# Kernel tuning notes

Measured on AMD Instinct MI355X. Metric: run time of the kernel, lower is better.

Reference implementation:

```python
import jax, jax.numpy as jnp
import numpy as np

N = 20000   # nodes
M = 20000   # hyperedges
E = 400000  # incidences
F = 256     # raw feature dim (exact_num_feature_dim)
HID = 256   # hidden
HEADS = 4
FS = HID // HEADS  # factor_size
OUT = 128


def setup_inputs() -> dict:
    key = jax.random.key(0)
    k = jax.random.split(key, 5)
    x = jax.random.normal(k[0], (N, F), jnp.float32)
    edge_index = jax.random.randint(k[1], (2, E), 0, M)  # row0: node idx, row1: hyperedge idx
    edge_weight = jax.random.uniform(k[2], (E,), jnp.float32)
    W_enc = jax.random.normal(k[3], (F, HID), jnp.float32) / np.sqrt(F).astype(np.float32)
    W_cls = jax.random.normal(k[4], (F * HEADS, OUT), jnp.float32) / np.sqrt(F * HEADS).astype(np.float32)
    return {"x": x, "edge_weight": edge_weight, "W_enc": W_enc, "W_cls": W_cls,
            "edge_index": edge_index}


def _segment_mean(vals, idx, num):
    # mean-aggregate rows of vals into `num` segments (torch get_xe_by_mean_agg)
    s = jax.ops.segment_sum(vals, idx, num_segments=num)
    c = jax.ops.segment_sum(jnp.ones((idx.shape[0], 1), vals.dtype), idx, num_segments=num)
    return s / jnp.maximum(c, 1.0)


def reference(x, edge_weight, W_enc, W_cls, edge_index):
    src = edge_index[0]  # node index per incidence
    he = edge_index[1]   # hyperedge index per incidence
    x0 = x

    # encoder + per-head softmax over factor dim (dropout is identity in eval mode)
    h = (x @ W_enc).reshape(N, HEADS, FS)
    h = jax.nn.softmax(h, axis=-1).reshape(N, HEADS * FS)

    # hyperedge embeddings = mean of member-node embeddings
    h_gather = h[src]                                    # [E, HID]
    temp_edge = _segment_mean(h_gather, he, M).reshape(M, HEADS, FS)
    temp_x = h_gather.reshape(E, HEADS, FS)

    # elementwise attention score per incidence, scatter-min per hyperedge
    att_calc = (temp_edge[he] * temp_x).sum(-1)          # [E, HEADS]
    att_score = jnp.full((M, HEADS), jnp.inf, h.dtype).at[he].min(att_calc)
    att_score = jnp.where(jnp.isinf(att_score), jnp.zeros((), h.dtype), att_score)

    # disentanglement factor loss
    gram = jnp.einsum('mhf,mgf->mhg', temp_edge, temp_edge)  # [M, HEADS, HEADS]
    factor_loss = (-(temp_edge * temp_edge).sum(-1) + jax.nn.logsumexp(gram, axis=-1)).mean()

    # propagation layer: node->hyperedge mean of raw feats, per-head attention scale,
    # then hyperedge->node mean; concat heads -> [N, HEADS*F]
    xe = _segment_mean(x0[src], he, M)                   # [M, F]
    xe_h = att_score[:, :, None] * xe[:, None, :]        # [M, HEADS, F]
    x_out = _segment_mean(xe_h[he].reshape(E, HEADS * F), src, N)  # [N, HEADS*F]

    logits = x_out @ W_cls                               # [N, OUT]
    return logits, factor_loss
```

## Files before the change

kernel.cpp:

```cpp
#include <hip/hip_runtime.h>
#include <hip/hip_fp16.h>

#define N_NODES 20000
#define M_EDGES 20000
#define E_INC   400000
#define HE_CACHE 8

__device__ __forceinline__ unsigned char f2e5(float f) {
  unsigned short u = __half_as_ushort(__float2half_rn(f));
  u = (unsigned short)(u + 0x7F + ((u >> 8) & 1));
  return (unsigned char)(u >> 8);
}
__device__ __forceinline__ float e52f(unsigned b) {
  return __half2float(__ushort_as_half((unsigned short)(b << 8)));
}
__device__ __forceinline__ float4 e5x4(unsigned p) {
  float4 r;
  r.x = e52f(p & 0xFFu);  r.y = e52f((p >> 8) & 0xFFu);
  r.z = e52f((p >> 16) & 0xFFu);  r.w = e52f(p >> 24);
  return r;
}

__global__ __launch_bounds__(256) void encode_kernel(
    const float* __restrict__ x, const float* __restrict__ Wenc,
    unsigned char* __restrict__ hx)
{
  __shared__ float xs[16][256];
  const int n0 = blockIdx.x * 16;
  const int t = threadIdx.x;
  #pragma unroll
  for (int r = 0; r < 16; ++r) xs[r][t] = x[(size_t)(n0 + r) * 256 + t];
  __syncthreads();

  float acc[16];
  #pragma unroll
  for (int r = 0; r < 16; ++r) acc[r] = 0.f;
  for (int k = 0; k < 256; k += 4) {
    float w0 = Wenc[(size_t)(k+0)*256 + t];
    float w1 = Wenc[(size_t)(k+1)*256 + t];
    float w2 = Wenc[(size_t)(k+2)*256 + t];
    float w3 = Wenc[(size_t)(k+3)*256 + t];
    #pragma unroll
    for (int r = 0; r < 16; ++r) {
      float4 xv = *(const float4*)&xs[r][k];
      acc[r] = fmaf(xv.x, w0, acc[r]);
      acc[r] = fmaf(xv.y, w1, acc[r]);
      acc[r] = fmaf(xv.z, w2, acc[r]);
      acc[r] = fmaf(xv.w, w3, acc[r]);
    }
  }
  const int chunk_off = (t >> 2) * 8 + (t & 3);
  #pragma unroll
  for (int r = 0; r < 16; ++r) {
    float v = acc[r];
    float mx = v;
    #pragma unroll
    for (int off = 32; off >= 1; off >>= 1) mx = fmaxf(mx, __shfl_xor(mx, off, 64));
    float ev = expf(v - mx);
    float sum = ev;
    #pragma unroll
    for (int off = 32; off >= 1; off >>= 1) sum += __shfl_xor(sum, off, 64);
    unsigned char* row = hx + (size_t)(n0 + r) * 512;
    row[chunk_off]     = f2e5(ev / sum);
    row[chunk_off + 4] = f2e5(xs[r][t]);
  }
}

__global__ __launch_bounds__(256) void hist_kernel(
    const int* __restrict__ src, const int* __restrict__ he,
    int* __restrict__ cnt_he, int* __restrict__ cnt_nd,
    int* __restrict__ rank_he, int* __restrict__ rank_nd)
{
  const int e = blockIdx.x * 256 + threadIdx.x;
  if (e >= E_INC) return;
  rank_he[e] = atomicAdd(&cnt_he[he[e]], 1);
  rank_nd[e] = atomicAdd(&cnt_nd[src[e]], 1);
}

__global__ __launch_bounds__(1024) void scan_kernel(
    const int* __restrict__ cnt_he, int* __restrict__ start_he,
    const int* __restrict__ cnt_nd, int* __restrict__ start_nd)
{
  const int* cnt = (blockIdx.x == 0) ? cnt_he : cnt_nd;
  int* start     = (blockIdx.x == 0) ? start_he : start_nd;
  const int n = 20000;
  __shared__ int sums[1024];
  const int t = threadIdx.x;
  const int base = t * 20;
  int local[20];
  int s = 0;
  #pragma unroll
  for (int j = 0; j < 20; ++j) {
    int idx = base + j;
    int v = (idx < n) ? cnt[idx] : 0;
    local[j] = s; s += v;
  }
  sums[t] = s; __syncthreads();
  for (int off = 1; off < 1024; off <<= 1) {
    int v = (t >= off) ? sums[t - off] : 0;
    __syncthreads();
    sums[t] += v;
    __syncthreads();
  }
  const int pre = (t > 0) ? sums[t - 1] : 0;
  #pragma unroll
  for (int j = 0; j < 20; ++j) {
    int idx = base + j;
    if (idx <= n) start[idx] = pre + local[j];
  }
}

__global__ __launch_bounds__(256) void bucket_kernel(
    const int* __restrict__ src, const int* __restrict__ he,
    const int* __restrict__ start_he, const int* __restrict__ start_nd,
    const int* __restrict__ rank_he, const int* __restrict__ rank_nd,
    int* __restrict__ list_he, int* __restrict__ list_nd)
{
  const int e = blockIdx.x * 256 + threadIdx.x;
  if (e >= E_INC) return;
  const int s = src[e], m = he[e];
  list_he[start_he[m] + rank_he[e]] = s;
  list_nd[start_nd[s] + rank_nd[e]] = m;
}

__global__ __launch_bounds__(256) void he_kernel(
    const unsigned char* __restrict__ hx,
    const int* __restrict__ start_he, const int* __restrict__ list_he,
    float* __restrict__ xe, float* __restrict__ att,
    float* __restrict__ loss_arr)
{
  const int m = blockIdx.x;
  const int t = threadIdx.x;
  const int wave = t >> 6, lane = t & 63;
  const int s0 = start_he[m], s1 = start_he[m + 1];
  const int deg = s1 - s0;
  __shared__ int mem[256];
  __shared__ __align__(16) float part[4][256];
  __shared__ __align__(16) float te_s[256];
  __shared__ float att_p[4][4];
  __shared__ float gram_s[16];

  const int cnt0 = min(deg, 256);
  if (t < cnt0) mem[t] = list_he[s0 + t];
  __syncthreads();

  float4 acch = {0.f,0.f,0.f,0.f}, accx = {0.f,0.f,0.f,0.f};
  unsigned cache[HE_CACHE];
  #pragma unroll
  for (int j = 0; j < HE_CACHE; ++j) {
    const int i = wave + 4 * j;
    unsigned hp = 0;
    if (i < cnt0) {
      const int s = mem[i];
      uint2 p = *(const uint2*)(hx + (size_t)s * 512 + 8 * lane);
      hp = p.x;
      float4 hv = e5x4(p.x), xv = e5x4(p.y);
      acch.x += hv.x; acch.y += hv.y; acch.z += hv.z; acch.w += hv.w;
      accx.x += xv.x; accx.y += xv.y; accx.z += xv.z; accx.w += xv.w;
    }
    cache[j] = hp;
  }
  for (int i = 32 + wave; i < cnt0; i += 4) {
    const int s = mem[i];
    uint2 p = *(const uint2*)(hx + (size_t)s * 512 + 8 * lane);
    float4 hv = e5x4(p.x), xv = e5x4(p.y);
    acch.x += hv.x; acch.y += hv.y; acch.z += hv.z; acch.w += hv.w;
    accx.x += xv.x; accx.y += xv.y; accx.z += xv.z; accx.w += xv.w;
  }
  for (int base = 256; base < deg; base += 256) {
    const int cnt = min(256, deg - base);
    __syncthreads();
    if (t < cnt) mem[t] = list_he[s0 + base + t];
    __syncthreads();
    for (int i = wave; i < cnt; i += 4) {
      const int s = mem[i];
      uint2 p = *(const uint2*)(hx + (size_t)s * 512 + 8 * lane);
      float4 hv = e5x4(p.x), xv = e5x4(p.y);
      acch.x += hv.x; acch.y += hv.y; acch.z += hv.z; acch.w += hv.w;
      accx.x += xv.x; accx.y += xv.y; accx.z += xv.z; accx.w += xv.w;
    }
  }

  const float inv = 1.0f / (float)(deg > 1 ? deg : 1);
  *(float4*)&part[wave][4 * lane] = acch;
  __syncthreads();
  te_s[t] = ((part[0][t] + part[1][t]) + (part[2][t] + part[3][t])) * inv;
  __syncthreads();
  *(float4*)&part[wave][4 * lane] = accx;
  __syncthreads();
  xe[(size_t)m * 256 + t] =
      ((part[0][t] + part[1][t]) + (part[2][t] + part[3][t])) * inv;

  const float4 tew = *(const float4*)&te_s[4 * lane];
  float amin = 3.4e38f;
  #pragma unroll
  for (int j = 0; j < HE_CACHE; ++j) {
    const int i = wave + 4 * j;
    if (i < cnt0) {
      const float4 hv = e5x4(cache[j]);
      float d = tew.x*hv.x + tew.y*hv.y + tew.z*hv.z + tew.w*hv.w;
      d += __shfl_xor(d, 1, 16);
      d += __shfl_xor(d, 2, 16);
      d += __shfl_xor(d, 4, 16);
      d += __shfl_xor(d, 8, 16);
      amin = fminf(amin, d);
    }
  }
  if (deg > 256) {
    __syncthreads();
    mem[t] = list_he[s0 + t];
    __syncthreads();
  }
  for (int i = 32 + wave; i < cnt0; i += 4) {
    const int s = mem[i];
    unsigned hp = *(const unsigned*)(hx + (size_t)s * 512 + 8 * lane);
    const float4 hv = e5x4(hp);
    float d = tew.x*hv.x + tew.y*hv.y + tew.z*hv.z + tew.w*hv.w;
    d += __shfl_xor(d, 1, 16);
    d += __shfl_xor(d, 2, 16);
    d += __shfl_xor(d, 4, 16);
    d += __shfl_xor(d, 8, 16);
    amin = fminf(amin, d);
  }
  for (int base = 256; base < deg; base += 256) {
    const int cnt = min(256, deg - base);
    __syncthreads();
    if (t < cnt) mem[t] = list_he[s0 + base + t];
    __syncthreads();
    for (int i = wave; i < cnt; i += 4) {
      const int s = mem[i];
      unsigned hp = *(const unsigned*)(hx + (size_t)s * 512 + 8 * lane);
      const float4 hv = e5x4(hp);
      float d = tew.x*hv.x + tew.y*hv.y + tew.z*hv.z + tew.w*hv.w;
      d += __shfl_xor(d, 1, 16);
      d += __shfl_xor(d, 2, 16);
      d += __shfl_xor(d, 4, 16);
      d += __shfl_xor(d, 8, 16);
      amin = fminf(amin, d);
    }
  }
  if ((lane & 15) == 0) att_p[wave][lane >> 4] = amin;
  __syncthreads();
  if (t < 4) {
    float a = fminf(fminf(att_p[0][t], att_p[1][t]),
                    fminf(att_p[2][t], att_p[3][t]));
    att[(size_t)m * 4 + t] = (a > 1e30f) ? 0.f : a;
  }

  if (t < 64) {
    const int pr = t >> 2, sub = t & 3;
    const int a = pr >> 2, b = pr & 3;
    const float* pa = &te_s[a * 64 + sub * 16];
    const float* pb = &te_s[b * 64 + sub * 16];
    float g = 0.f;
    #pragma unroll
    for (int f = 0; f < 16; ++f) g += pa[f] * pb[f];
    g += __shfl_xor(g, 1, 4);
    g += __shfl_xor(g, 2, 4);
    if (sub == 0) gram_s[pr] = g;
  }
  __syncthreads();
  if (t == 0) {
    float lsum = 0.f;
    #pragma unroll
    for (int hh = 0; hh < 4; ++hh) {
      float g0 = gram_s[hh*4+0], g1 = gram_s[hh*4+1];
      float g2 = gram_s[hh*4+2], g3 = gram_s[hh*4+3];
      float mx = fmaxf(fmaxf(g0, g1), fmaxf(g2, g3));
      float se = expf(g0-mx) + expf(g1-mx) + expf(g2-mx) + expf(g3-mx);
      lsum += -gram_s[hh*4+hh] + mx + logf(se);
    }
    loss_arr[m] = lsum;
  }
}

__global__ __launch_bounds__(256) void z_kernel(
    const float* __restrict__ xe, const float* __restrict__ att,
    const float* __restrict__ Wcls, unsigned char* __restrict__ zb)
{
  __shared__ float xs[16][256];
  __shared__ float as[16][4];
  const int m0 = blockIdx.x * 16;
  const int t = threadIdx.x;
  const int o = t & 127;
  const int half = t >> 7;
  for (int i = t; i < 1024; i += 256)
    ((float4*)&xs[0][0])[i] = ((const float4*)(xe + (size_t)m0 * 256))[i];
  if (t < 64) ((float*)as)[t] = att[(size_t)m0 * 4 + t];
  __syncthreads();

  float acc[8][4] = {};
  for (int f4 = 0; f4 < 64; ++f4) {
    float4 xv[8];
    #pragma unroll
    for (int r = 0; r < 8; ++r) xv[r] = *(const float4*)&xs[half * 8 + r][f4 * 4];
    #pragma unroll
    for (int hh = 0; hh < 4; ++hh) {
      #pragma unroll
      for (int j = 0; j < 4; ++j) {
        float w = Wcls[(size_t)(hh*256 + f4*4 + j) * 128 + o];
        #pragma unroll
        for (int r = 0; r < 8; ++r)
          acc[r][hh] = fmaf(((const float*)&xv[r])[j], w, acc[r][hh]);
      }
    }
  }
  #pragma unroll
  for (int r = 0; r < 8; ++r) {
    const int row = half * 8 + r;
    float zv = as[row][0]*acc[r][0] + as[row][1]*acc[r][1]
             + as[row][2]*acc[r][2] + as[row][3]*acc[r][3];
    zb[(size_t)(m0 + row) * 128 + o] = f2e5(zv);
  }
}

__global__ __launch_bounds__(256) void node_kernel(
    const unsigned char* __restrict__ zb, const int* __restrict__ start_nd,
    const int* __restrict__ list_nd, float* __restrict__ out)
{
  const int n = blockIdx.x * 4 + (threadIdx.x >> 6);
  const int lane = threadIdx.x & 63;
  const int g = lane >> 5, l32 = lane & 31;
  const int s0 = start_nd[n], s1 = start_nd[n + 1];
  const int deg = s1 - s0;
  float4 acc = {0.f, 0.f, 0.f, 0.f};
  for (int base = s0; base < s1; base += 64) {
    const int cnt = min(64, s1 - base);
    const int mi = (lane < cnt) ? list_nd[base + lane] : 0;
    for (int i = g; i < cnt; i += 2) {
      const int mm = __shfl(mi, i);
      const unsigned v = *(const unsigned*)(zb + (size_t)mm * 128 + 4 * l32);
      const float4 f = e5x4(v);
      acc.x += f.x; acc.y += f.y; acc.z += f.z; acc.w += f.w;
    }
  }
  acc.x += __shfl_xor(acc.x, 32);
  acc.y += __shfl_xor(acc.y, 32);
  acc.z += __shfl_xor(acc.z, 32);
  acc.w += __shfl_xor(acc.w, 32);
  if (lane < 32) {
    const float inv = 1.0f / (float)(deg > 1 ? deg : 1);
    float4 o;
    o.x = acc.x * inv; o.y = acc.y * inv;
    o.z = acc.z * inv; o.w = acc.w * inv;
    *(float4*)(out + (size_t)n * 128 + 4 * l32) = o;
  }
}

__global__ __launch_bounds__(1024) void reduce_loss_kernel(
    const float* __restrict__ loss_arr, float* __restrict__ out)
{
  __shared__ float sums[1024];
  const int t = threadIdx.x;
  float s = 0.f;
  for (int i = t; i < M_EDGES; i += 1024) s += loss_arr[i];
  sums[t] = s; __syncthreads();
  for (int off = 512; off >= 1; off >>= 1) {
    if (t < off) sums[t] += sums[t + off];
    __syncthreads();
  }
  if (t == 0) out[(size_t)N_NODES * 128] = sums[0] / (float)(M_EDGES * 4);
}

extern "C" void kernel_launch(void* const* d_in, const int* in_sizes, int n_in,
                              void* d_out, int out_size, void* d_ws, size_t ws_size,
                              hipStream_t stream)
{
  const float* x    = (const float*)d_in[0];
  const float* Wenc = (const float*)d_in[2];
  const float* Wcls = (const float*)d_in[3];
  const int*   ei   = (const int*)d_in[4];
  const int*   src  = ei;
  const int*   he   = ei + E_INC;
  float* out = (float*)d_out;

  char* ws = (char*)d_ws;
  unsigned char* hx = (unsigned char*)(ws);
  float* xe       = (float*)(ws + 10240000);
  unsigned char* zb = (unsigned char*)(ws + 30720000);
  float* att      = (float*)(ws + 33280000);
  int*   cnt_he   = (int*)  (ws + 33600000);
  int*   cnt_nd   = (int*)  (ws + 33680000);
  int*   rank_he  = (int*)  (ws + 33760000);
  int*   rank_nd  = (int*)  (ws + 35360000);
  int*   start_he = (int*)  (ws + 36960000);
  int*   start_nd = (int*)  (ws + 37040064);
  int*   list_he  = (int*)  (ws + 37120128);
  int*   list_nd  = (int*)  (ws + 38720128);
  float* loss_arr = (float*)(ws + 40320128);

  hipMemsetAsync(cnt_he, 0, 160000, stream);

  encode_kernel     <<<1250,  256, 0, stream>>>(x, Wenc, hx);
  hist_kernel       <<<1563,  256, 0, stream>>>(src, he, cnt_he, cnt_nd,
                                                rank_he, rank_nd);
  scan_kernel       <<<2,    1024, 0, stream>>>(cnt_he, start_he, cnt_nd, start_nd);
  bucket_kernel     <<<1563,  256, 0, stream>>>(src, he, start_he, start_nd,
                                                rank_he, rank_nd, list_he, list_nd);
  he_kernel         <<<20000, 256, 0, stream>>>(hx, start_he, list_he,
                                                xe, att, loss_arr);
  z_kernel          <<<1250,  256, 0, stream>>>(xe, att, Wcls, zb);
  node_kernel       <<<5000,  256, 0, stream>>>(zb, start_nd, list_nd, out);
  reduce_loss_kernel<<<1,    1024, 0, stream>>>(loss_arr, out);
}
```

Baseline: 367.3 us.

## Run hyperedge classifier projection on bf16 MFMA with bf16 xe storage

Replaces the scalar FP32 z_kernel with an MFMA-based kernel that uses bf16 16x16x32 matrix instructions. Hyperedge mean features xe are stored as bf16 instead of fp32, and W_cls is transposed and converted to bf16 by a new small kernel each call. This targets the FP32 FMA cost of the [M,256]x[256,512] projection and halves xe memory traffic. The trade-off is lower precision in xe and W, plus an extra launch.

```diff
diff --git a/kernel.cpp b/kernel.cpp
--- a/kernel.cpp
+++ b/kernel.cpp
@@ -5,6 +5,9 @@
 #define M_EDGES 20000
 #define E_INC   400000
 #define HE_CACHE 8
+
+using bf16x8 = __attribute__((ext_vector_type(8))) __bf16;
+using f32x4  = __attribute__((ext_vector_type(4))) float;
 
 __device__ __forceinline__ unsigned char f2e5(float f) {
   unsigned short u = __half_as_ushort(__float2half_rn(f));
@@ -19,6 +22,11 @@
   r.x = e52f(p & 0xFFu);  r.y = e52f((p >> 8) & 0xFFu);
   r.z = e52f((p >> 16) & 0xFFu);  r.w = e52f(p >> 24);
   return r;
+}
+__device__ __forceinline__ unsigned short f2bf(float f) {
+  unsigned u = __float_as_uint(f);
+  u += 0x7FFF + ((u >> 16) & 1);
+  return (unsigned short)(u >> 16);
 }
 
 __global__ __launch_bounds__(256) void encode_kernel(
@@ -66,6 +74,15 @@
   }
 }
 
+__global__ __launch_bounds__(256) void cvt_w_kernel(
+    const float* __restrict__ Wcls, unsigned short* __restrict__ Wt)
+{
+  const int c = blockIdx.x;
+  const int t = threadIdx.x;
+  Wt[(size_t)c * 256 + t] =
+      f2bf(Wcls[(size_t)((c >> 7) * 256 + t) * 128 + (c & 127)]);
+}
+
 __global__ __launch_bounds__(256) void hist_kernel(
     const int* __restrict__ src, const int* __restrict__ he,
     int* __restrict__ cnt_he, int* __restrict__ cnt_nd,
@@ -126,7 +143,7 @@
 __global__ __launch_bounds__(256) void he_kernel(
     const unsigned char* __restrict__ hx,
     const int* __restrict__ start_he, const int* __restrict__ list_he,
-    float* __restrict__ xe, float* __restrict__ att,
+    unsigned short* __restrict__ xe_b, float* __restrict__ att,
     float* __restrict__ loss_arr)
 {
   const int m = blockIdx.x;
@@ -188,8 +205,8 @@
   __syncthreads();
   *(float4*)&part[wave][4 * lane] = accx;
   __syncthreads();
-  xe[(size_t)m * 256 + t] =
-      ((part[0][t] + part[1][t]) + (part[2][t] + part[3][t])) * inv;
+  xe_b[(size_t)m * 256 + t] =
+      f2bf(((part[0][t] + part[1][t]) + (part[2][t] + part[3][t])) * inv);
 
   const float4 tew = *(const float4*)&te_s[4 * lane];
   float amin = 3.4e38f;
@@ -274,43 +291,49 @@
   }
 }
 
-__global__ __launch_bounds__(256) void z_kernel(
-    const float* __restrict__ xe, const float* __restrict__ att,
-    const float* __restrict__ Wcls, unsigned char* __restrict__ zb)
-{
-  __shared__ float xs[16][256];
-  __shared__ float as[16][4];
-  const int m0 = blockIdx.x * 16;
-  const int t = threadIdx.x;
-  const int o = t & 127;
-  const int half = t >> 7;
-  for (int i = t; i < 1024; i += 256)
-    ((float4*)&xs[0][0])[i] = ((const float4*)(xe + (size_t)m0 * 256))[i];
-  if (t < 64) ((float*)as)[t] = att[(size_t)m0 * 4 + t];
-  __syncthreads();
-
-  float acc[8][4] = {};
-  for (int f4 = 0; f4 < 64; ++f4) {
-    float4 xv[8];
-    #pragma unroll
-    for (int r = 0; r < 8; ++r) xv[r] = *(const float4*)&xs[half * 8 + r][f4 * 4];
-    #pragma unroll
-    for (int hh = 0; hh < 4; ++hh) {
+__global__ __launch_bounds__(256) void z_mfma_kernel(
+    const unsigned short* __restrict__ xe_b, const unsigned short* __restrict__ Wt,
+    const float* __restrict__ att, unsigned char* __restrict__ zb)
+{
+  const int t = threadIdx.x;
+  const int w = t >> 6, l = t & 63;
+  const int m0 = blockIdx.x * 32;
+  __shared__ float att_s[32][4];
+  if (t < 128) att_s[t >> 2][t & 3] = att[(size_t)(m0 + (t >> 2)) * 4 + (t & 3)];
+  __syncthreads();
+
+  f32x4 acc[2][2][4] = {};
+  const int arow0 = (size_t)(m0 + (l & 15)) * 256 + (l >> 4) * 8;
+  const int brow  = (size_t)(w * 32 + (l & 15)) * 256 + (l >> 4) * 8;
+  for (int ks = 0; ks < 8; ++ks) {
+    const int k0 = ks * 32;
+    bf16x8 a0 = *(const bf16x8*)(xe_b + arow0 + k0);
+    bf16x8 a1 = *(const bf16x8*)(xe_b + arow0 + 16 * 256 + k0);
+    #pragma unroll
+    for (int h = 0; h < 4; ++h) {
       #pragma unroll
-      for (int j = 0; j < 4; ++j) {
-        float w = Wcls[(size_t)(hh*256 + f4*4 + j) * 128 + o];
-        #pragma unroll
-        for (int r = 0; r < 8; ++r)
-          acc[r][hh] = fmaf(((const float*)&xv[r])[j], w, acc[r][hh]);
+      for (int ct = 0; ct < 2; ++ct) {
+        bf16x8 b = *(const bf16x8*)(Wt + brow + (size_t)(h * 128 + ct * 16) * 256 + k0);
+        acc[0][ct][h] = __builtin_amdgcn_mfma_f32_16x16x32_bf16(a0, b, acc[0][ct][h], 0, 0, 0);
+        acc[1][ct][h] = __builtin_amdgcn_mfma_f32_16x16x32_bf16(a1, b, acc[1][ct][h], 0, 0, 0);
       }
     }
   }
-  #pragma unroll
-  for (int r = 0; r < 8; ++r) {
-    const int row = half * 8 + r;
-    float zv = as[row][0]*acc[r][0] + as[row][1]*acc[r][1]
-             + as[row][2]*acc[r][2] + as[row][3]*acc[r][3];
-    zb[(size_t)(m0 + row) * 128 + o] = f2e5(zv);
+
+  #pragma unroll
+  for (int rt = 0; rt < 2; ++rt) {
+    #pragma unroll
+    for (int j = 0; j < 4; ++j) {
+      const int row_local = rt * 16 + (l >> 4) * 4 + j;
+      const float a0_ = att_s[row_local][0], a1_ = att_s[row_local][1];
+      const float a2_ = att_s[row_local][2], a3_ = att_s[row_local][3];
+      #pragma unroll
+      for (int ct = 0; ct < 2; ++ct) {
+        float zv = a0_ * acc[rt][ct][0][j] + a1_ * acc[rt][ct][1][j]
+                 + a2_ * acc[rt][ct][2][j] + a3_ * acc[rt][ct][3][j];
+        zb[(size_t)(m0 + row_local) * 128 + w * 32 + ct * 16 + (l & 15)] = f2e5(zv);
+      }
+    }
   }
 }
 
@@ -375,22 +398,24 @@
   float* out = (float*)d_out;
 
   char* ws = (char*)d_ws;
-  unsigned char* hx = (unsigned char*)(ws);
-  float* xe       = (float*)(ws + 10240000);
-  unsigned char* zb = (unsigned char*)(ws + 30720000);
-  float* att      = (float*)(ws + 33280000);
-  int*   cnt_he   = (int*)  (ws + 33600000);
-  int*   cnt_nd   = (int*)  (ws + 33680000);
-  int*   rank_he  = (int*)  (ws + 33760000);
-  int*   rank_nd  = (int*)  (ws + 35360000);
-  int*   start_he = (int*)  (ws + 36960000);
-  int*   start_nd = (int*)  (ws + 37040064);
-  int*   list_he  = (int*)  (ws + 37120128);
-  int*   list_nd  = (int*)  (ws + 38720128);
-  float* loss_arr = (float*)(ws + 40320128);
+  unsigned char*  hx   = (unsigned char*)(ws);
+  unsigned short* xe_b = (unsigned short*)(ws + 10240000);
+  unsigned char*  zb   = (unsigned char*)(ws + 20480000);
+  float* att      = (float*)(ws + 23040000);
+  unsigned short* Wt = (unsigned short*)(ws + 23360000);
+  int*   cnt_he   = (int*)  (ws + 23700000);
+  int*   cnt_nd   = (int*)  (ws + 23780000);
+  int*   rank_he  = (int*)  (ws + 23860000);
+  int*   rank_nd  = (int*)  (ws + 25460000);
+  int*   start_he = (int*)  (ws + 27060000);
+  int*   start_nd = (int*)  (ws + 27140064);
+  int*   list_he  = (int*)  (ws + 27220128);
+  int*   list_nd  = (int*)  (ws + 28820128);
+  float* loss_arr = (float*)(ws + 30420128);
 
   hipMemsetAsync(cnt_he, 0, 160000, stream);
 
+  cvt_w_kernel      <<<512,   256, 0, stream>>>(Wcls, Wt);
   encode_kernel     <<<1250,  256, 0, stream>>>(x, Wenc, hx);
   hist_kernel       <<<1563,  256, 0, stream>>>(src, he, cnt_he, cnt_nd,
                                                 rank_he, rank_nd);
@@ -398,8 +423,8 @@
   bucket_kernel     <<<1563,  256, 0, stream>>>(src, he, start_he, start_nd,
                                                 rank_he, rank_nd, list_he, list_nd);
   he_kernel         <<<20000, 256, 0, stream>>>(hx, start_he, list_he,
-                                                xe, att, loss_arr);
-  z_kernel          <<<1250,  256, 0, stream>>>(xe, att, Wcls, zb);
+                                                xe_b, att, loss_arr);
+  z_mfma_kernel     <<<625,   256, 0, stream>>>(xe_b, Wt, att, zb);
   node_kernel       <<<5000,  256, 0, stream>>>(zb, start_nd, list_nd, out);
   reduce_loss_kernel<<<1,    1024, 0, stream>>>(loss_arr, out);
 }
```

Result: faster. 325.6 us (-11.4%).
